# Kernel tuning notes

Hardware: AMD Instinct MI355X
Metric: run time of the kernel (lower is better)

Reference implementation:

```python
import jax, jax.numpy as jnp
import numpy as np

N = 10000
E = 320000
D = 256


def setup_inputs() -> dict:
    key = jax.random.key(0)
    ks = jax.random.split(key, 10)
    s = 1.0 / np.sqrt(D)
    return {
        "x0": jax.random.normal(ks[0], (N, D), jnp.float32),
        "edge_index": jax.random.randint(ks[1], (2, E), 0, N, jnp.int32),
        "W1": jax.random.normal(ks[2], (D, D), jnp.float32) * s,
        "b1": jax.random.normal(ks[3], (D,), jnp.float32) * s,
        "W2": jax.random.normal(ks[4], (D, D), jnp.float32) * s,
        "b2": jax.random.normal(ks[5], (D,), jnp.float32) * s,
        "wa1": jax.random.normal(ks[6], (D,), jnp.float32) * s,
        "ba1": jax.random.normal(ks[7], (1,), jnp.float32) * s,
        "wa2": jax.random.normal(ks[8], (D,), jnp.float32) * s,
        "ba2": jax.random.normal(ks[9], (1,), jnp.float32) * s,
    }


def reference(x0, edge_index, W1, b1, W2, b2, wa1, ba1, wa2, ba2):
    n = x0.shape[0]
    leaky = lambda v: jax.nn.leaky_relu(v, 0.2)
    x0_i = leaky(x0 @ W1 + b1)                      # [N, D]
    x0_j = leaky(x0 @ W2 + b2)                      # [N, D]
    a1 = x0_i @ wa1 + ba1[0]                        # [N]
    a2 = x0_j @ wa2 + ba2[0]                        # [N]
    row, col = edge_index[0], edge_index[1]
    # sigmoid(a_1 + a_2.T)[row, col] without the dense N x N intermediate
    att = jax.nn.sigmoid(a1[row] + a2[col])         # [E]
    msg = att[:, None] * x0_j[col]                  # [E, D]
    out = jax.ops.segment_sum(msg, row, num_segments=n)  # sparse.mm(attention, x0_j)
    return out + x0
```

## Files before the change

kernel.cpp:

```cpp
#include <hip/hip_runtime.h>
#include <math.h>

#define D 256
#define CAP 128
#define APAD 264

typedef float f32x4 __attribute__((ext_vector_type(4)));
typedef short s16x8 __attribute__((ext_vector_type(8)));
typedef unsigned short u16x8 __attribute__((ext_vector_type(8)));

static __device__ __forceinline__ unsigned short f2bf(float x) {
    union { float f; unsigned u; } v; v.f = x;
    unsigned r = v.u + 0x7fff + ((v.u >> 16) & 1);
    return (unsigned short)(r >> 16);
}

__global__ __launch_bounds__(256) void k_init(
    const float* __restrict__ W1, const float* __restrict__ W2,
    unsigned short* __restrict__ wt, int* __restrict__ curp, int n)
{
    const int i = blockIdx.x * 256 + threadIdx.x;
    if (i < 2 * D * D) {
        int k = i >> 9;
        int j = i & 511;
        float v = (j < D) ? W1[(size_t)k * D + j] : W2[(size_t)k * D + (j - D)];
        wt[(size_t)j * D + k] = f2bf(v);
    }
    if (i < n) curp[(size_t)i << 5] = 0;
}

__global__ __launch_bounds__(1024) void k_mfma_rank(
    const float* __restrict__ x0, const unsigned short* __restrict__ wt,
    const float* __restrict__ b1, const float* __restrict__ b2,
    const float* __restrict__ wa1, const float* __restrict__ wa2,
    const float* __restrict__ ba1, const float* __restrict__ ba2,
    const int* __restrict__ rows, const int* __restrict__ cols,
    int* __restrict__ curp, unsigned short* __restrict__ perm,
    unsigned char* __restrict__ x0j8, float* __restrict__ a1,
    float2* __restrict__ a2s, int n, int e, int nrb)
{
    __shared__ unsigned short Atile[32][APAD];
    __shared__ float part[16][32];
    __shared__ float pmx[8][32];
    __shared__ float sscale[32];
    const int t = threadIdx.x;

    if ((int)blockIdx.x < nrb) {
        const int i0 = (blockIdx.x * 1024 + t) * 8;
        if (i0 + 7 < e) {
            int4 ra = *(const int4*)&rows[i0];
            int4 rb4 = *(const int4*)&rows[i0 + 4];
            int4 ca = *(const int4*)&cols[i0];
            int4 cb4 = *(const int4*)&cols[i0 + 4];
            int s0 = atomicAdd(&curp[(size_t)ra.x << 5], 1);
            int s1 = atomicAdd(&curp[(size_t)ra.y << 5], 1);
            int s2 = atomicAdd(&curp[(size_t)ra.z << 5], 1);
            int s3 = atomicAdd(&curp[(size_t)ra.w << 5], 1);
            int s4 = atomicAdd(&curp[(size_t)rb4.x << 5], 1);
            int s5 = atomicAdd(&curp[(size_t)rb4.y << 5], 1);
            int s6 = atomicAdd(&curp[(size_t)rb4.z << 5], 1);
            int s7 = atomicAdd(&curp[(size_t)rb4.w << 5], 1);
            if (s0 < CAP) perm[(size_t)ra.x * CAP + s0] = (unsigned short)ca.x;
            if (s1 < CAP) perm[(size_t)ra.y * CAP + s1] = (unsigned short)ca.y;
            if (s2 < CAP) perm[(size_t)ra.z * CAP + s2] = (unsigned short)ca.z;
            if (s3 < CAP) perm[(size_t)ra.w * CAP + s3] = (unsigned short)ca.w;
            if (s4 < CAP) perm[(size_t)rb4.x * CAP + s4] = (unsigned short)cb4.x;
            if (s5 < CAP) perm[(size_t)rb4.y * CAP + s5] = (unsigned short)cb4.y;
            if (s6 < CAP) perm[(size_t)rb4.z * CAP + s6] = (unsigned short)cb4.z;
            if (s7 < CAP) perm[(size_t)rb4.w * CAP + s7] = (unsigned short)cb4.w;
        } else {
            for (int i = i0; i < e; ++i) {
                int r = rows[i];
                int slot = atomicAdd(&curp[(size_t)r << 5], 1);
                if (slot < CAP) perm[(size_t)r * CAP + slot] = (unsigned short)cols[i];
            }
        }
        return;
    }

    const int lane = t & 63, w = t >> 6;
    const int rb = (blockIdx.x - nrb) * 32;
    const int lr = lane & 15;
    const int kg = lane >> 4;

    {
        const int row = t >> 5, seg = t & 31;
        int gr = rb + row; if (gr >= n) gr = n - 1;
        f32x4 v0 = *(const f32x4*)&x0[(size_t)gr * D + seg * 8];
        f32x4 v1 = *(const f32x4*)&x0[(size_t)gr * D + seg * 8 + 4];
        u16x8 o;
        o[0] = f2bf(v0.x); o[1] = f2bf(v0.y); o[2] = f2bf(v0.z); o[3] = f2bf(v0.w);
        o[4] = f2bf(v1.x); o[5] = f2bf(v1.y); o[6] = f2bf(v1.z); o[7] = f2bf(v1.w);
        *(u16x8*)&Atile[row][seg * 8] = o;
    }
    __syncthreads();

    const int cb = w * 32;
    f32x4 acc[2][2] = {};

    #pragma unroll
    for (int ks = 0; ks < 8; ++ks) {
        const int k0 = ks * 32 + kg * 8;
        s16x8 af[2];
        af[0] = *(const s16x8*)&Atile[lr][k0];
        af[1] = *(const s16x8*)&Atile[16 + lr][k0];
        s16x8 bfr[2];
        #pragma unroll
        for (int cf = 0; cf < 2; ++cf)
            bfr[cf] = *(const s16x8*)&wt[(size_t)(cb + cf * 16 + lr) * D + k0];
        #pragma unroll
        for (int rf = 0; rf < 2; ++rf)
            #pragma unroll
            for (int cf = 0; cf < 2; ++cf)
                acc[rf][cf] = __builtin_amdgcn_mfma_f32_16x16x32_bf16(
                    af[rf], bfr[cf], acc[rf][cf], 0, 0, 0);
    }

    const bool isW2 = (w >= 8);
    const float* wav  = isW2 ? wa2 : wa1;
    const float* bias = isW2 ? b2  : b1;
    const int crel = cb - (isW2 ? D : 0);

    float bvv[2], wvv[2];
    #pragma unroll
    for (int cf = 0; cf < 2; ++cf) {
        bvv[cf] = bias[crel + cf * 16 + lr];
        wvv[cf] = wav[crel + cf * 16 + lr];
    }

    float rs[2][4] = {};
    float mx[2][4] = {};
    #pragma unroll
    for (int rf = 0; rf < 2; ++rf)
        #pragma unroll
        for (int cf = 0; cf < 2; ++cf)
            #pragma unroll
            for (int r = 0; r < 4; ++r) {
                float v = acc[rf][cf][r] + bvv[cf];
                v = (v > 0.0f) ? v : 0.2f * v;
                rs[rf][r] += v * wvv[cf];
                mx[rf][r] = fmaxf(mx[rf][r], fabsf(v));
            }

    #pragma unroll
    for (int rf = 0; rf < 2; ++rf)
        #pragma unroll
        for (int r = 0; r < 4; ++r) {
            float s = rs[rf][r], m = mx[rf][r];
            #pragma unroll
            for (int o = 1; o < 16; o <<= 1) {
                s += __shfl_xor(s, o, 64);
                m = fmaxf(m, __shfl_xor(m, o, 64));
            }
            if (lr == 0) {
                const int ri = rf * 16 + kg * 4 + r;
                part[w][ri] = s;
                if (isW2) pmx[w - 8][ri] = m;
            }
        }
    __syncthreads();
    if (t < 32) {
        const int row = rb + t;
        float s1v = 0.0f, s2v = 0.0f, smax = 1e-20f;
        #pragma unroll
        for (int ww = 0; ww < 8; ++ww) {
            s1v += part[ww][t];
            s2v += part[8 + ww][t];
            smax = fmaxf(smax, pmx[ww][t]);
        }
        float sc = smax * (1.0f / 127.0f);
        sscale[t] = sc;
        if (row < n) {
            a1[row] = s1v + ba1[0] + ba2[0];
            float2 av; av.x = s2v; av.y = sc;
            a2s[row] = av;
        }
    }
    __syncthreads();

    if (isW2) {
        #pragma unroll
        for (int rf = 0; rf < 2; ++rf)
            #pragma unroll
            for (int r = 0; r < 4; ++r) {
                const int ri = rf * 16 + kg * 4 + r;
                const int row = rb + ri;
                if (row >= n) continue;
                const float inv_s = 1.0f / sscale[ri];
                #pragma unroll
                for (int cf = 0; cf < 2; ++cf) {
                    const int col = crel + cf * 16 + lr;
                    float v = acc[rf][cf][r] + bvv[cf];
                    v = (v > 0.0f) ? v : 0.2f * v;
                    int qv = (int)rintf(v * inv_s) + 128;
                    qv = (qv < 0) ? 0 : ((qv > 255) ? 255 : qv);
                    x0j8[(size_t)row * D + col] = (unsigned char)qv;
                }
            }
    }
}

__global__ __launch_bounds__(256) void k_agg(
    const unsigned char* __restrict__ x0j8, const float* __restrict__ x0,
    const float* __restrict__ a1, const float2* __restrict__ a2s,
    const int* __restrict__ curp, const unsigned short* __restrict__ perm,
    float* __restrict__ out, int n)
{
    __shared__ unsigned short scol[4][CAP + 4];
    __shared__ float satt[4][CAP + 4];

    const int w = threadIdx.x >> 6, lane = threadIdx.x & 63;
    const int q = lane >> 4, hl = lane & 15;
    const int row = blockIdx.x * 4 + w;

    int deg = 0;
    f32x4 res;
    if (row < n) {
        deg = curp[(size_t)row << 5];
        if (deg > CAP) deg = CAP;
        const size_t pbase = (size_t)row * CAP;
        const float a1r = a1[row];
        res = *(const f32x4*)&x0[(size_t)row * D + hl * 16 + q * 4];

        for (int i = lane; i < deg; i += 64) {
            int c = perm[pbase + i];
            scol[w][i] = (unsigned short)c;
            float2 p = a2s[c];
            float att = 1.0f / (1.0f + __expf(-(a1r + p.x)));
            satt[w][i] = att * p.y;
        }
        if (lane < 4) {
            scol[w][deg + lane] = 0;
            satt[w][deg + lane] = 0.0f;
        }
    }
    __syncthreads();
    if (row >= n) return;

    const int degp = (deg + 3) & ~3;

    float acc[16];
    #pragma unroll
    for (int k = 0; k < 16; ++k) acc[k] = 0.0f;
    float corr = 0.0f;

    #pragma unroll 2
    for (int j = 0; j < degp; j += 4) {
        const int idx = j + q;
        const float as = satt[w][idx];
        const int   c  = scol[w][idx];
        uint4 v = *(const uint4*)&x0j8[(size_t)c * D + hl * 16];
        corr += as;
        acc[0]  += as * (float)( v.x        & 255);
        acc[1]  += as * (float)((v.x >>  8) & 255);
        acc[2]  += as * (float)((v.x >> 16) & 255);
        acc[3]  += as * (float)( v.x >> 24);
        acc[4]  += as * (float)( v.y        & 255);
        acc[5]  += as * (float)((v.y >>  8) & 255);
        acc[6]  += as * (float)((v.y >> 16) & 255);
        acc[7]  += as * (float)( v.y >> 24);
        acc[8]  += as * (float)( v.z        & 255);
        acc[9]  += as * (float)((v.z >>  8) & 255);
        acc[10] += as * (float)((v.z >> 16) & 255);
        acc[11] += as * (float)( v.z >> 24);
        acc[12] += as * (float)( v.w        & 255);
        acc[13] += as * (float)((v.w >>  8) & 255);
        acc[14] += as * (float)((v.w >> 16) & 255);
        acc[15] += as * (float)( v.w >> 24);
    }

    #pragma unroll
    for (int k = 0; k < 16; ++k) acc[k] += __shfl_xor(acc[k], 16, 64);
    corr += __shfl_xor(corr, 16, 64);
    #pragma unroll
    for (int k = 0; k < 16; ++k) acc[k] += __shfl_xor(acc[k], 32, 64);
    corr += __shfl_xor(corr, 32, 64);

    const float bias128 = 128.0f * corr;

    float s0, s1, s2, s3;
    if      (q == 0) { s0 = acc[0];  s1 = acc[1];  s2 = acc[2];  s3 = acc[3];  }
    else if (q == 1) { s0 = acc[4];  s1 = acc[5];  s2 = acc[6];  s3 = acc[7];  }
    else if (q == 2) { s0 = acc[8];  s1 = acc[9];  s2 = acc[10]; s3 = acc[11]; }
    else             { s0 = acc[12]; s1 = acc[13]; s2 = acc[14]; s3 = acc[15]; }

    const int col = hl * 16 + q * 4;
    f32x4 o;
    o.x = res.x + s0 - bias128;
    o.y = res.y + s1 - bias128;
    o.z = res.z + s2 - bias128;
    o.w = res.w + s3 - bias128;
    *(f32x4*)&out[(size_t)row * D + col] = o;
}

extern "C" void kernel_launch(void* const* d_in, const int* in_sizes, int n_in,
                              void* d_out, int out_size, void* d_ws, size_t ws_size,
                              hipStream_t stream)
{
    const float* x0  = (const float*)d_in[0];
    const int*   ei  = (const int*)d_in[1];
    const float* W1  = (const float*)d_in[2];
    const float* b1  = (const float*)d_in[3];
    const float* W2  = (const float*)d_in[4];
    const float* b2  = (const float*)d_in[5];
    const float* wa1 = (const float*)d_in[6];
    const float* ba1 = (const float*)d_in[7];
    const float* wa2 = (const float*)d_in[8];
    const float* ba2 = (const float*)d_in[9];
    float* out = (float*)d_out;

    const int n = in_sizes[0] / D;
    const int e = in_sizes[1] / 2;
    const int* rows = ei;
    const int* cols = ei + e;

    char* ws = (char*)d_ws;
    unsigned short* wt   = (unsigned short*)ws;
    unsigned char*  x0j8 = (unsigned char*)(wt + (size_t)2 * D * D);
    float*  a1   = (float*)(x0j8 + (size_t)n * D);
    float2* a2s  = (float2*)(a1 + n);
    int*    curp = (int*)(a2s + n);
    unsigned short* perm = (unsigned short*)(curp + (size_t)n * 32);

    const int ithreads = 2 * D * D;
    k_init<<<(ithreads + 255) / 256, 256, 0, stream>>>(W1, W2, wt, curp, n);
    const int gx = (n + 31) / 32;
    const int nrb = (e / 8 + 1023) / 1024;
    k_mfma_rank<<<nrb + gx, 1024, 0, stream>>>(x0, wt, b1, b2, wa1, wa2,
                                               ba1, ba2, rows, cols, curp, perm,
                                               x0j8, a1, a2s, n, e, nrb);
    k_agg<<<(n + 3) / 4, 256, 0, stream>>>(x0j8, x0, a1, a2s, curp, perm, out, n);
}
```

Before: 62.18 us.

## Split fused GEMM block into two 512-thread blocks per row tile for W1/W2

The 1024-thread block that computed both W1 and W2 projections for a 32-row tile becomes two 512-thread blocks, one per weight matrix, and the edge-bucketing blocks are resized to match. Smaller blocks should give the scheduler more blocks to distribute across CUs and allow better occupancy. In exchange, each 32-row x0 tile is loaded and converted to bf16 twice.

```diff
diff --git a/kernel.cpp b/kernel.cpp
--- a/kernel.cpp
+++ b/kernel.cpp
@@ -29,7 +29,7 @@
     if (i < n) curp[(size_t)i << 5] = 0;
 }
 
-__global__ __launch_bounds__(1024) void k_mfma_rank(
+__global__ __launch_bounds__(512) void k_mfma_rank(
     const float* __restrict__ x0, const unsigned short* __restrict__ wt,
     const float* __restrict__ b1, const float* __restrict__ b2,
     const float* __restrict__ wa1, const float* __restrict__ wa2,
@@ -40,13 +40,13 @@
     float2* __restrict__ a2s, int n, int e, int nrb)
 {
     __shared__ unsigned short Atile[32][APAD];
-    __shared__ float part[16][32];
+    __shared__ float part[8][32];
     __shared__ float pmx[8][32];
     __shared__ float sscale[32];
     const int t = threadIdx.x;
 
     if ((int)blockIdx.x < nrb) {
-        const int i0 = (blockIdx.x * 1024 + t) * 8;
+        const int i0 = (blockIdx.x * 512 + t) * 8;
         if (i0 + 7 < e) {
             int4 ra = *(const int4*)&rows[i0];
             int4 rb4 = *(const int4*)&rows[i0 + 4];
@@ -79,12 +79,14 @@
     }
 
     const int lane = t & 63, w = t >> 6;
-    const int rb = (blockIdx.x - nrb) * 32;
+    const int bid2 = blockIdx.x - nrb;
+    const int bx = bid2 >> 1, by = bid2 & 1;
+    const int rb = bx * 32;
     const int lr = lane & 15;
     const int kg = lane >> 4;
 
-    {
-        const int row = t >> 5, seg = t & 31;
+    for (int s = t; s < 1024; s += 512) {
+        const int row = s >> 5, seg = s & 31;
         int gr = rb + row; if (gr >= n) gr = n - 1;
         f32x4 v0 = *(const f32x4*)&x0[(size_t)gr * D + seg * 8];
         f32x4 v1 = *(const f32x4*)&x0[(size_t)gr * D + seg * 8 + 4];
@@ -95,9 +97,10 @@
     }
     __syncthreads();
 
-    const int cb = w * 32;
+    const int cl = w * 32;
+    const int wrow0 = by * D + cl;
+
     f32x4 acc[2][2] = {};
-
     #pragma unroll
     for (int ks = 0; ks < 8; ++ks) {
         const int k0 = ks * 32 + kg * 8;
@@ -107,7 +110,7 @@
         s16x8 bfr[2];
         #pragma unroll
         for (int cf = 0; cf < 2; ++cf)
-            bfr[cf] = *(const s16x8*)&wt[(size_t)(cb + cf * 16 + lr) * D + k0];
+            bfr[cf] = *(const s16x8*)&wt[(size_t)(wrow0 + cf * 16 + lr) * D + k0];
         #pragma unroll
         for (int rf = 0; rf < 2; ++rf)
             #pragma unroll
@@ -116,16 +119,14 @@
                     af[rf], bfr[cf], acc[rf][cf], 0, 0, 0);
     }
 
-    const bool isW2 = (w >= 8);
-    const float* wav  = isW2 ? wa2 : wa1;
-    const float* bias = isW2 ? b2  : b1;
-    const int crel = cb - (isW2 ? D : 0);
+    const float* wav  = by ? wa2 : wa1;
+    const float* bias = by ? b2  : b1;
 
     float bvv[2], wvv[2];
     #pragma unroll
     for (int cf = 0; cf < 2; ++cf) {
-        bvv[cf] = bias[crel + cf * 16 + lr];
-        wvv[cf] = wav[crel + cf * 16 + lr];
+        bvv[cf] = bias[cl + cf * 16 + lr];
+        wvv[cf] = wav[cl + cf * 16 + lr];
     }
 
     float rs[2][4] = {};
@@ -155,30 +156,32 @@
             if (lr == 0) {
                 const int ri = rf * 16 + kg * 4 + r;
                 part[w][ri] = s;
-                if (isW2) pmx[w - 8][ri] = m;
+                pmx[w][ri] = m;
             }
         }
     __syncthreads();
     if (t < 32) {
         const int row = rb + t;
-        float s1v = 0.0f, s2v = 0.0f, smax = 1e-20f;
+        float sv = 0.0f, smax = 1e-20f;
         #pragma unroll
         for (int ww = 0; ww < 8; ++ww) {
-            s1v += part[ww][t];
-            s2v += part[8 + ww][t];
+            sv += part[ww][t];
             smax = fmaxf(smax, pmx[ww][t]);
         }
         float sc = smax * (1.0f / 127.0f);
         sscale[t] = sc;
         if (row < n) {
-            a1[row] = s1v + ba1[0] + ba2[0];
-            float2 av; av.x = s2v; av.y = sc;
-            a2s[row] = av;
+            if (by == 0) {
+                a1[row] = sv + ba1[0] + ba2[0];
+            } else {
+                float2 av; av.x = sv; av.y = sc;
+                a2s[row] = av;
+            }
         }
     }
     __syncthreads();
 
-    if (isW2) {
+    if (by == 1) {
         #pragma unroll
         for (int rf = 0; rf < 2; ++rf)
             #pragma unroll
@@ -189,7 +192,7 @@
                 const float inv_s = 1.0f / sscale[ri];
                 #pragma unroll
                 for (int cf = 0; cf < 2; ++cf) {
-                    const int col = crel + cf * 16 + lr;
+                    const int col = cl + cf * 16 + lr;
                     float v = acc[rf][cf][r] + bvv[cf];
                     v = (v > 0.0f) ? v : 0.2f * v;
                     int qv = (int)rintf(v * inv_s) + 128;
@@ -324,9 +327,9 @@
 
     const int ithreads = 2 * D * D;
     k_init<<<(ithreads + 255) / 256, 256, 0, stream>>>(W1, W2, wt, curp, n);
-    const int gx = (n + 31) / 32;
-    const int nrb = (e / 8 + 1023) / 1024;
-    k_mfma_rank<<<nrb + gx, 1024, 0, stream>>>(x0, wt, b1, b2, wa1, wa2,
+    const int gx2 = ((n + 31) / 32) * 2;
+    const int nrb = (e / 8 + 511) / 512;
+    k_mfma_rank<<<nrb + gx2, 512, 0, stream>>>(x0, wt, b1, b2, wa1, wa2,
                                                ba1, ba2, rows, cols, curp, perm,
                                                x0j8, a1, a2s, n, e, nrb);
     k_agg<<<(n + 3) / 4, 256, 0, stream>>>(x0j8, x0, a1, a2s, curp, perm, out, n);
```

Result: faster. 54.81 us (-11.9%).
